# Kernel tuning notes

Measured on AMD Instinct MI355X. Metric: run time of the kernel, lower is better.

The kernel has to match this reference:

```python
import jax, jax.numpy as jnp
import numpy as np

B, S, HID = 1, 2048, 4096
NH, KVH, D = 32, 8, 128
MAXP = 2048
EPS = 1e-6


def _rope_tables(max_pos, dim, base=10000.0):
    inv_freq = 1.0 / (base ** (np.arange(0, dim, 2, dtype=np.float32) / dim))
    t = np.arange(max_pos, dtype=np.float32)
    freqs = np.outer(t, inv_freq)                      # [max_pos, dim/2]
    emb = np.concatenate([freqs, freqs], axis=-1)      # [max_pos, dim]
    return jnp.asarray(np.cos(emb)), jnp.asarray(np.sin(emb))


def setup_inputs() -> dict:
    key = jax.random.key(0)
    ks = jax.random.split(key, 6)
    x = jax.random.normal(ks[0], (B, S, HID), jnp.float32)
    scale = 0.02
    wq = jax.random.normal(ks[1], (NH * D, HID), jnp.float32) * scale
    wk = jax.random.normal(ks[2], (KVH * D, HID), jnp.float32) * scale
    wv = jax.random.normal(ks[3], (KVH * D, HID), jnp.float32) * scale
    wo = jax.random.normal(ks[4], (NH * D, HID), jnp.float32).T * scale  # stored as [HID, NH*D] -> transpose back
    wo = jnp.asarray(jax.random.normal(ks[4], (HID, NH * D), jnp.float32) * scale)
    cos_table, sin_table = _rope_tables(MAXP, D)
    return {
        "x": x, "wq": wq, "wk": wk, "wv": wv, "wo": wo,
        "q_norm_w": jnp.ones((D,), jnp.float32),
        "k_norm_w": jnp.ones((D,), jnp.float32),
        "cos_table": cos_table, "sin_table": sin_table,
        "k_cache": jnp.zeros((1, B, MAXP, KVH, D), jnp.float32),
        "v_cache": jnp.zeros((1, B, MAXP, KVH, D), jnp.float32),
        "positions": jnp.arange(S, dtype=jnp.int32),
        "layer_idx": 0,
    }


def _rmsnorm(x, w):
    return w * (x * jax.lax.rsqrt(jnp.mean(x * x, axis=-1, keepdims=True) + EPS))


def _rope(x, cos, sin):
    # x: [B, H, S, D]; cos/sin: [1, 1, S, D]
    half = x.shape[-1] // 2
    x1, x2 = x[..., :half], x[..., half:]
    rotated = jnp.concatenate([-x2, x1], axis=-1)
    return x * cos + rotated * sin


def reference(x, wq, wk, wv, wo, q_norm_w, k_norm_w, cos_table, sin_table,
              k_cache, v_cache, positions, layer_idx):
    bsz, seq_len, _ = x.shape
    d = q_norm_w.shape[0]
    nh = wq.shape[0] // d
    kvh = wk.shape[0] // d
    g = nh // kvh

    q = (x @ wq.T).reshape(bsz, seq_len, nh, d).transpose(0, 2, 1, 3)    # [B,NH,S,D]
    k = (x @ wk.T).reshape(bsz, seq_len, kvh, d).transpose(0, 2, 1, 3)   # [B,KVH,S,D]
    v = (x @ wv.T).reshape(bsz, seq_len, kvh, d).transpose(0, 2, 1, 3)

    q = _rmsnorm(q, q_norm_w)
    k = _rmsnorm(k, k_norm_w)

    cos = cos_table[positions][None, None]  # [1,1,S,D]
    sin = sin_table[positions][None, None]
    q = _rope(q, cos, sin)
    k = _rope(k, cos, sin)

    # KV-cache scatter at dynamic positions (prefill: positions = arange(S))
    kc = k_cache[layer_idx].at[:, positions].set(k.transpose(0, 2, 1, 3))
    vc = v_cache[layer_idx].at[:, positions].set(v.transpose(0, 2, 1, 3))
    # K = max(positions)+1 == seq_len in this (prefill) setup; static for jit
    K = seq_len
    k_all = kc[:, :K].transpose(0, 2, 1, 3)   # [B,KVH,K,D]
    v_all = vc[:, :K].transpose(0, 2, 1, 3)

    # GQA: group query heads instead of repeat_interleave on K/V (same math)
    qg = q.reshape(bsz, kvh, g, seq_len, d)
    scale = 1.0 / jnp.sqrt(jnp.asarray(d, q.dtype))
    scores = jnp.einsum('bkgqd,bkld->bkgql', qg, k_all) * scale
    causal = jnp.tril(jnp.ones((seq_len, K), dtype=bool))
    scores = jnp.where(causal, scores, jnp.finfo(scores.dtype).min)
    attn = jax.nn.softmax(scores, axis=-1)
    out = jnp.einsum('bkgql,bkld->bkgqd', attn, v_all)
    out = out.reshape(bsz, nh, seq_len, d).transpose(0, 2, 1, 3).reshape(bsz, seq_len, nh * d)
    return out @ wo.T
```

## Files before the change

kernel.cpp:

```cpp
#include <hip/hip_runtime.h>

typedef unsigned short u16;
typedef unsigned int u32;
typedef __attribute__((ext_vector_type(8))) short bf16x8;
typedef __attribute__((ext_vector_type(4))) float f32x4;
struct __align__(8) us4 { u16 x, y, z, w; };

#define S_LEN 2048
#define HID   4096
#define NH    32
#define KVH   8
#define HD    128
#define QP_ELEMS (S_LEN * HID)

__device__ inline u16 f2bf(float f) {
  u32 u = __float_as_uint(f);
  u32 r = (u + 0x7fffu + ((u >> 16) & 1u)) >> 16;
  return (u16)r;
}
__device__ inline float bf2f(u16 h) { return __uint_as_float(((u32)h) << 16); }

__device__ inline void gld_lds16(const void* g, void* l) {
  __builtin_amdgcn_global_load_lds(
      (const __attribute__((address_space(1))) u32*)g,
      (__attribute__((address_space(3))) u32*)l, 16, 0, 0);
}

__global__ __launch_bounds__(256)
void cvt_all(const float* __restrict__ x, const float* __restrict__ wq,
             const float* __restrict__ wk, const float* __restrict__ wv,
             const float* __restrict__ wo, u16* __restrict__ xb,
             u16* __restrict__ wqb, u16* __restrict__ wkb,
             u16* __restrict__ wvb, u16* __restrict__ wob) {
  int b = blockIdx.x;
  const float* in; u16* out; int base;
  if (b < 8192)       { in = x;  out = xb;  base = b; }
  else if (b < 24576) { in = wq; out = wqb; base = b - 8192; }
  else if (b < 28672) { in = wk; out = wkb; base = b - 24576; }
  else if (b < 32768) { in = wv; out = wvb; base = b - 28672; }
  else                { in = wo; out = wob; base = b - 32768; }
  size_t i = ((size_t)base * 256 + threadIdx.x) * 4;
  f32x4 v = *(const f32x4*)(in + i);
  us4 o;
  o.x = f2bf(v[0]); o.y = f2bf(v[1]); o.z = f2bf(v[2]); o.w = f2bf(v[3]);
  *(us4*)(out + i) = o;
}

__device__ inline void gemm_core_128(const u16* __restrict__ A,
                                     const u16* __restrict__ W,
                                     int m0, int n0, int K,
                                     int kStart, int kEnd,
                                     u16* lA, u16* lB, f32x4 (&acc)[4][4]) {
  const int t = threadIdx.x;
  const int l = t & 63, w = t >> 6;
  const int quad = l >> 4, l15 = l & 15;
  const int wr = w >> 1, wc = w & 1;
  const int srow = t >> 2;
  const int scol = (t & 3) * 8;
#pragma unroll
  for (int i = 0; i < 4; i++)
#pragma unroll
    for (int j = 0; j < 4; j++) acc[i][j] = (f32x4){0.f, 0.f, 0.f, 0.f};

  for (int k0 = kStart; k0 < kEnd; k0 += 32) {
    gld_lds16(A + (size_t)(m0 + srow) * K + k0 + scol, lA + srow * 32 + scol);
    gld_lds16(A + (size_t)(m0 + 64 + srow) * K + k0 + scol, lA + (64 + srow) * 32 + scol);
    gld_lds16(W + (size_t)(n0 + srow) * K + k0 + scol, lB + srow * 32 + scol);
    gld_lds16(W + (size_t)(n0 + 64 + srow) * K + k0 + scol, lB + (64 + srow) * 32 + scol);
    __syncthreads();
    bf16x8 af[4], bfr[4];
#pragma unroll
    for (int i = 0; i < 4; i++)
      af[i] = *(const bf16x8*)(lA + (wr * 64 + i * 16 + l15) * 32 + quad * 8);
#pragma unroll
    for (int j = 0; j < 4; j++)
      bfr[j] = *(const bf16x8*)(lB + (wc * 64 + j * 16 + l15) * 32 + quad * 8);
#pragma unroll
    for (int i = 0; i < 4; i++)
#pragma unroll
      for (int j = 0; j < 4; j++)
        acc[i][j] = __builtin_amdgcn_mfma_f32_16x16x32_bf16(af[i], bfr[j], acc[i][j], 0, 0, 0);
    __syncthreads();
  }
}

__global__ __launch_bounds__(256, 3)
void gemm_qkv(const u16* __restrict__ xb, const u16* __restrict__ wqb,
              const u16* __restrict__ wkb, const u16* __restrict__ wvb,
              u16* __restrict__ Qp, u16* __restrict__ Kp, u16* __restrict__ vt) {
  __shared__ __align__(16) u16 lA[128 * 32];
  __shared__ __align__(16) u16 lB[128 * 32];
  const int bx = blockIdx.x;
  const int m0 = blockIdx.y * 128;
  const u16* W; u16* C; int n0, ldc, epi;
  if (bx < 32)      { W = wqb; C = Qp; n0 = bx * 128;        ldc = HID;  epi = 0; }
  else if (bx < 40) { W = wkb; C = Kp; n0 = (bx - 32) * 128; ldc = 1024; epi = 0; }
  else              { W = wvb; C = vt; n0 = (bx - 40) * 128; ldc = 0;    epi = 1; }

  f32x4 acc[4][4];
  gemm_core_128(xb, W, m0, n0, HID, 0, HID, lA, lB, acc);

  const int t = threadIdx.x, l = t & 63, w = t >> 6;
  const int quad = l >> 4, l15 = l & 15;
  const int wr = w >> 1, wc = w & 1;
  if (epi == 0) {
#pragma unroll
    for (int i = 0; i < 4; i++) {
      int row0 = m0 + wr * 64 + i * 16 + quad * 4;
#pragma unroll
      for (int j = 0; j < 4; j++) {
        int col = n0 + wc * 64 + j * 16 + l15;
#pragma unroll
        for (int r = 0; r < 4; r++)
          C[(size_t)(row0 + r) * ldc + col] = f2bf(acc[i][j][r]);
      }
    }
  } else {
#pragma unroll
    for (int i = 0; i < 4; i++) {
      int row0 = m0 + wr * 64 + i * 16 + quad * 4;
#pragma unroll
      for (int j = 0; j < 4; j++) {
        int col = n0 + wc * 64 + j * 16 + l15;
        us4 v;
        v.x = f2bf(acc[i][j][0]); v.y = f2bf(acc[i][j][1]);
        v.z = f2bf(acc[i][j][2]); v.w = f2bf(acc[i][j][3]);
        *(us4*)(C + (size_t)col * S_LEN + row0) = v;
      }
    }
  }
}

__global__ __launch_bounds__(256, 3)
void gemm_out(const u16* __restrict__ ab, const u16* __restrict__ wob,
              u16* __restrict__ Po) {
  __shared__ __align__(16) u16 lA[128 * 32];
  __shared__ __align__(16) u16 lB[128 * 32];
  const int m0 = blockIdx.y * 128, n0 = blockIdx.x * 128;
  const int z = blockIdx.z;
  const int kStart = z * 1376;
  const int kEnd = (z == 2) ? HID : kStart + 1376;
  u16* C = Po + (size_t)z * QP_ELEMS;
  f32x4 acc[4][4];
  gemm_core_128(ab, wob, m0, n0, HID, kStart, kEnd, lA, lB, acc);
  const int t = threadIdx.x, l = t & 63, w = t >> 6;
  const int quad = l >> 4, l15 = l & 15;
  const int wr = w >> 1, wc = w & 1;
#pragma unroll
  for (int i = 0; i < 4; i++) {
    int row0 = m0 + wr * 64 + i * 16 + quad * 4;
#pragma unroll
    for (int j = 0; j < 4; j++) {
      int col = n0 + wc * 64 + j * 16 + l15;
#pragma unroll
      for (int r = 0; r < 4; r++)
        C[(size_t)(row0 + r) * HID + col] = f2bf(acc[i][j][r]);
    }
  }
}

__global__ __launch_bounds__(256)
void reduce_out(const u16* __restrict__ Po, float* __restrict__ outp) {
  size_t i = ((size_t)blockIdx.x * 256 + threadIdx.x) * 4;
  us4 a = *(const us4*)(Po + i);
  us4 b = *(const us4*)(Po + QP_ELEMS + i);
  us4 c = *(const us4*)(Po + 2 * QP_ELEMS + i);
  f32x4 o;
  o[0] = bf2f(a.x) + bf2f(b.x) + bf2f(c.x);
  o[1] = bf2f(a.y) + bf2f(b.y) + bf2f(c.y);
  o[2] = bf2f(a.z) + bf2f(b.z) + bf2f(c.z);
  o[3] = bf2f(a.w) + bf2f(b.w) + bf2f(c.w);
  *(f32x4*)(outp + i) = o;
}

__global__ __launch_bounds__(256)
void rope_all(const u16* __restrict__ Qp, const u16* __restrict__ Kp,
              const float* __restrict__ qnw, const float* __restrict__ knw,
              const float* __restrict__ cosT, const float* __restrict__ sinT,
              const int* __restrict__ pos, u16* __restrict__ qbh,
              u16* __restrict__ kbh) {
  const int b = blockIdx.x;
  const int t = threadIdx.x, w = t >> 6, l = t & 63;
  const u16* xr; const float* nw; u16* orow; int s;
  if (b < 16384) {
    int p = b * 4 + w;
    s = p >> 5; int h = p & 31;
    xr = Qp + (size_t)s * HID + h * HD;
    nw = qnw;
    orow = qbh + ((size_t)h * S_LEN + s) * HD;
  } else {
    int p = (b - 16384) * 4 + w;
    s = p >> 3; int h = p & 7;
    xr = Kp + (size_t)s * 1024 + h * HD;
    nw = knw;
    orow = kbh + ((size_t)h * S_LEN + s) * HD;
  }
  float x1 = bf2f(xr[l]);
  float x2 = bf2f(xr[l + 64]);
  float ss = x1 * x1 + x2 * x2;
#pragma unroll
  for (int m = 1; m < 64; m <<= 1) ss += __shfl_xor(ss, m);
  float rinv = rsqrtf(ss * (1.0f / 128.0f) + 1e-6f);
  float n1 = x1 * rinv * nw[l];
  float n2 = x2 * rinv * nw[l + 64];
  int ps = pos[s];
  float c1 = cosT[ps * HD + l], s1 = sinT[ps * HD + l];
  float c2 = cosT[ps * HD + l + 64], s2 = sinT[ps * HD + l + 64];
  float y1 = n1 * c1 - n2 * s1;
  float y2 = n2 * c2 + n1 * s2;
  orow[l] = f2bf(y1);
  orow[l + 64] = f2bf(y2);
}

__global__ __launch_bounds__(256)
void attn_fwd(const u16* __restrict__ qh, const u16* __restrict__ kbh,
              const u16* __restrict__ vth, u16* __restrict__ ab) {
  __shared__ __align__(16) u16 lK[64 * 128];
  __shared__ __align__(16) u16 lV[128 * 64];
  __shared__ __align__(16) u16 lP[4][16 * 72];
  const int t = threadIdx.x, w = t >> 6, l = t & 63;
  const int quad = l >> 4, l15 = l & 15;
  const int h = blockIdx.x;
  const int qt = 31 - blockIdx.y;
  const int kvh = h >> 2;
  const int q0 = qt * 64;
  const int qrow = q0 + w * 16 + l15;

  bf16x8 qf[4];
#pragma unroll
  for (int ks = 0; ks < 4; ks++)
    qf[ks] = *(const bf16x8*)(qh + ((size_t)h * S_LEN + qrow) * HD + ks * 32 + quad * 8);

  f32x4 accO[8];
#pragma unroll
  for (int j = 0; j < 8; j++) accO[j] = (f32x4){0.f, 0.f, 0.f, 0.f};
  float m_cur = -3.0e38f, l_sum = 0.f;
  const float scale2 = 0.12751743f;

  const int ntiles = qt + 1;
  for (int tt = 0; tt < ntiles; tt++) {
    const int c0 = tt * 64;
#pragma unroll
    for (int i = 0; i < 4; i++) {
      int Cc = i * 256 + t;
      int r = Cc >> 4, ch = Cc & 15;
      int gch = ch ^ (r & 15);
      gld_lds16(kbh + ((size_t)kvh * S_LEN + c0 + r) * HD + gch * 8, lK + Cc * 8);
    }
#pragma unroll
    for (int i = 0; i < 4; i++) {
      int Cc = i * 256 + t;
      int d = Cc >> 3, ch = Cc & 7;
      int gch = ch ^ (d & 7);
      gld_lds16(vth + ((size_t)kvh * HD + d) * S_LEN + c0 + gch * 8, lV + Cc * 8);
    }
    __syncthreads();

    f32x4 st[4];
#pragma unroll
    for (int i = 0; i < 4; i++) {
      f32x4 sa = (f32x4){0.f, 0.f, 0.f, 0.f};
      int r = i * 16 + l15;
#pragma unroll
      for (int ks = 0; ks < 4; ks++) {
        int lc = ks * 4 + quad;
        bf16x8 kf = *(const bf16x8*)(lK + r * 128 + ((lc ^ (r & 15)) * 8));
        sa = __builtin_amdgcn_mfma_f32_16x16x32_bf16(kf, qf[ks], sa, 0, 0, 0);
      }
      st[i] = sa;
    }

    const bool needMask = (c0 + 63) > (q0 + w * 16);
    float tmax = -3.0e38f;
    if (needMask) {
#pragma unroll
      for (int i = 0; i < 4; i++) {
#pragma unroll
        for (int r = 0; r < 4; r++) {
          int kcol = c0 + i * 16 + quad * 4 + r;
          float v = st[i][r] * scale2;
          v = (kcol <= qrow) ? v : -3.0e38f;
          st[i][r] = v;
          tmax = fmaxf(tmax, v);
        }
      }
    } else {
#pragma unroll
      for (int i = 0; i < 4; i++) {
#pragma unroll
        for (int r = 0; r < 4; r++) {
          float v = st[i][r] * scale2;
          st[i][r] = v;
          tmax = fmaxf(tmax, v);
        }
      }
    }
    tmax = fmaxf(tmax, __shfl_xor(tmax, 16));
    tmax = fmaxf(tmax, __shfl_xor(tmax, 32));
    float m_new = fmaxf(m_cur, tmax);
    float alpha = exp2f(m_cur - m_new);

    float psum = 0.f;
#pragma unroll
    for (int i = 0; i < 4; i++) {
      us4 pv;
      u16* pp = (u16*)&pv;
#pragma unroll
      for (int r = 0; r < 4; r++) {
        float pe = exp2f(st[i][r] - m_new);
        psum += pe;
        pp[r] = f2bf(pe);
      }
      *(us4*)(&lP[w][l15 * 72 + i * 16 + quad * 4]) = pv;
    }
    psum += __shfl_xor(psum, 16);
    psum += __shfl_xor(psum, 32);
    l_sum = l_sum * alpha + psum;
    m_cur = m_new;

#pragma unroll
    for (int r = 0; r < 4; r++) {
      float ar = __shfl(alpha, quad * 4 + r);
#pragma unroll
      for (int j = 0; j < 8; j++) accO[j][r] *= ar;
    }

    bf16x8 pf[2];
#pragma unroll
    for (int ks = 0; ks < 2; ks++)
      pf[ks] = *(const bf16x8*)(&lP[w][l15 * 72 + ks * 32 + quad * 8]);
#pragma unroll
    for (int j = 0; j < 8; j++) {
      int d = j * 16 + l15;
#pragma unroll
      for (int ks = 0; ks < 2; ks++) {
        int lc = ks * 4 + quad;
        bf16x8 vf = *(const bf16x8*)(lV + d * 64 + ((lc ^ (d & 7)) * 8));
        accO[j] = __builtin_amdgcn_mfma_f32_16x16x32_bf16(pf[ks], vf, accO[j], 0, 0, 0);
      }
    }
    __syncthreads();
  }

  float linv = 1.0f / l_sum;
#pragma unroll
  for (int r = 0; r < 4; r++) {
    float lr = __shfl(linv, quad * 4 + r);
    int row = q0 + w * 16 + quad * 4 + r;
#pragma unroll
    for (int j = 0; j < 8; j++) {
      int col = h * HD + j * 16 + l15;
      ab[(size_t)row * HID + col] = f2bf(accO[j][r] * lr);
    }
  }
}

extern "C" void kernel_launch(void* const* d_in, const int* in_sizes, int n_in,
                              void* d_out, int out_size, void* d_ws, size_t ws_size,
                              hipStream_t stream) {
  const float* x    = (const float*)d_in[0];
  const float* wq   = (const float*)d_in[1];
  const float* wk   = (const float*)d_in[2];
  const float* wv   = (const float*)d_in[3];
  const float* wo   = (const float*)d_in[4];
  const float* qnw  = (const float*)d_in[5];
  const float* knw  = (const float*)d_in[6];
  const float* cosT = (const float*)d_in[7];
  const float* sinT = (const float*)d_in[8];
  const int* positions = (const int*)d_in[11];

  char* ws = (char*)d_ws;
  const size_t MB = 1048576ULL;
  u16* xb  = (u16*)(ws + 0 * MB);
  u16* wqb = (u16*)(ws + 16 * MB);
  u16* wkb = (u16*)(ws + 48 * MB);
  u16* wvb = (u16*)(ws + 56 * MB);
  u16* wob = (u16*)(ws + 64 * MB);
  u16* Qp  = (u16*)(ws + 96 * MB);
  u16* Kp  = (u16*)(ws + 112 * MB);
  u16* vt  = (u16*)(ws + 116 * MB);
  u16* qbh = (u16*)(ws + 120 * MB);
  u16* kbh = (u16*)(ws + 136 * MB);
  u16* ab  = (u16*)(ws + 140 * MB);
  u16* Po  = (u16*)(ws + 0 * MB);

  cvt_all<<<49152, 256, 0, stream>>>(x, wq, wk, wv, wo, xb, wqb, wkb, wvb, wob);

  gemm_qkv<<<dim3(48, 16), 256, 0, stream>>>(xb, wqb, wkb, wvb, Qp, Kp, vt);

  rope_all<<<20480, 256, 0, stream>>>(Qp, Kp, qnw, knw, cosT, sinT, positions,
                                      qbh, kbh);

  attn_fwd<<<dim3(NH, S_LEN / 64), 256, 0, stream>>>(qbh, kbh, vt, ab);

  gemm_out<<<dim3(HID / 128, S_LEN / 128, 3), 256, 0, stream>>>(ab, wob, Po);
  reduce_out<<<8192, 256, 0, stream>>>(Po, (float*)d_out);
}
```

Before: 541.8 us.

## Double query rows per attention block to reuse K/V tiles across two MFMA sets

Each warp in the attention kernel now handles 32 query rows instead of 16, so a block covers a 128-row query tile and every K/V tile loaded into LDS feeds twice as many MFMAs. The grid shrinks to 512 one-dimensional blocks, and the query-tile order interleaves long and short causal rows so block lengths are spread out. The accumulator rescale is skipped when no lane's running max changed, and launch bounds ask for two blocks per CU. The cost is more accumulator registers per thread and fewer blocks to hide latency, and the diagonal tiles now do more masked wasted work.

Result: slower. 552.8 us (+2.0%).

```diff
diff --git a/kernel.cpp b/kernel.cpp
--- a/kernel.cpp
+++ b/kernel.cpp
@@ -212,145 +212,157 @@
   orow[l + 64] = f2bf(y2);
 }
 
-__global__ __launch_bounds__(256)
+__global__ __launch_bounds__(256, 2)
 void attn_fwd(const u16* __restrict__ qh, const u16* __restrict__ kbh,
               const u16* __restrict__ vth, u16* __restrict__ ab) {
   __shared__ __align__(16) u16 lK[64 * 128];
   __shared__ __align__(16) u16 lV[128 * 64];
-  __shared__ __align__(16) u16 lP[4][16 * 72];
+  __shared__ __align__(16) u16 lP[4][32 * 72];
   const int t = threadIdx.x, w = t >> 6, l = t & 63;
   const int quad = l >> 4, l15 = l & 15;
-  const int h = blockIdx.x;
-  const int qt = 31 - blockIdx.y;
+  const int h = blockIdx.x & 31;
+  const int iz = blockIdx.x >> 5;
+  const int qt = (iz < 8) ? (15 - iz) : (iz - 8);
   const int kvh = h >> 2;
-  const int q0 = qt * 64;
-  const int qrow = q0 + w * 16 + l15;
-
-  bf16x8 qf[4];
-#pragma unroll
-  for (int ks = 0; ks < 4; ks++)
-    qf[ks] = *(const bf16x8*)(qh + ((size_t)h * S_LEN + qrow) * HD + ks * 32 + quad * 8);
-
-  f32x4 accO[8];
-#pragma unroll
-  for (int j = 0; j < 8; j++) accO[j] = (f32x4){0.f, 0.f, 0.f, 0.f};
-  float m_cur = -3.0e38f, l_sum = 0.f;
+  const int q0 = qt * 128;
+  const int qb = q0 + w * 32;
+
+  bf16x8 qf[2][4];
+#pragma unroll
+  for (int nt = 0; nt < 2; nt++)
+#pragma unroll
+    for (int ks = 0; ks < 4; ks++)
+      qf[nt][ks] = *(const bf16x8*)(qh + ((size_t)h * S_LEN + qb + nt * 16 + l15) * HD +
+                                    ks * 32 + quad * 8);
+
+  f32x4 accO[2][8];
+#pragma unroll
+  for (int nt = 0; nt < 2; nt++)
+#pragma unroll
+    for (int j = 0; j < 8; j++) accO[nt][j] = (f32x4){0.f, 0.f, 0.f, 0.f};
+  float m_cur[2] = {-3.0e38f, -3.0e38f}, l_sum[2] = {0.f, 0.f};
   const float scale2 = 0.12751743f;
 
-  const int ntiles = qt + 1;
+  const int ntiles = 2 * qt + 2;
   for (int tt = 0; tt < ntiles; tt++) {
     const int c0 = tt * 64;
 #pragma unroll
     for (int i = 0; i < 4; i++) {
       int Cc = i * 256 + t;
       int r = Cc >> 4, ch = Cc & 15;
-      int gch = ch ^ (r & 15);
-      gld_lds16(kbh + ((size_t)kvh * S_LEN + c0 + r) * HD + gch * 8, lK + Cc * 8);
+      gld_lds16(kbh + ((size_t)kvh * S_LEN + c0 + r) * HD + (ch ^ (r & 15)) * 8, lK + Cc * 8);
     }
 #pragma unroll
     for (int i = 0; i < 4; i++) {
       int Cc = i * 256 + t;
       int d = Cc >> 3, ch = Cc & 7;
-      int gch = ch ^ (d & 7);
-      gld_lds16(vth + ((size_t)kvh * HD + d) * S_LEN + c0 + gch * 8, lV + Cc * 8);
+      gld_lds16(vth + ((size_t)kvh * HD + d) * S_LEN + c0 + (ch ^ (d & 7)) * 8, lV + Cc * 8);
     }
     __syncthreads();
 
-    f32x4 st[4];
+    f32x4 st[2][4];
 #pragma unroll
     for (int i = 0; i < 4; i++) {
-      f32x4 sa = (f32x4){0.f, 0.f, 0.f, 0.f};
+      f32x4 s0 = (f32x4){0.f, 0.f, 0.f, 0.f};
+      f32x4 s1 = (f32x4){0.f, 0.f, 0.f, 0.f};
       int r = i * 16 + l15;
 #pragma unroll
       for (int ks = 0; ks < 4; ks++) {
-        int lc = ks * 4 + quad;
-        bf16x8 kf = *(const bf16x8*)(lK + r * 128 + ((lc ^ (r & 15)) * 8));
-        sa = __builtin_amdgcn_mfma_f32_16x16x32_bf16(kf, qf[ks], sa, 0, 0, 0);
-      }
-      st[i] = sa;
-    }
-
-    const bool needMask = (c0 + 63) > (q0 + w * 16);
-    float tmax = -3.0e38f;
-    if (needMask) {
+        bf16x8 kf = *(const bf16x8*)(lK + r * 128 + (((ks * 4 + quad) ^ (r & 15)) * 8));
+        s0 = __builtin_amdgcn_mfma_f32_16x16x32_bf16(kf, qf[0][ks], s0, 0, 0, 0);
+        s1 = __builtin_amdgcn_mfma_f32_16x16x32_bf16(kf, qf[1][ks], s1, 0, 0, 0);
+      }
+      st[0][i] = s0; st[1][i] = s1;
+    }
+
+#pragma unroll
+    for (int nt = 0; nt < 2; nt++) {
+      const int qrow = qb + nt * 16 + l15;
+      const bool needMask = (c0 + 63) > (qb + nt * 16);
+      float tmax = -3.0e38f;
+      if (needMask) {
+#pragma unroll
+        for (int i = 0; i < 4; i++)
+#pragma unroll
+          for (int r = 0; r < 4; r++) {
+            int kcol = c0 + i * 16 + quad * 4 + r;
+            float v = st[nt][i][r] * scale2;
+            v = (kcol <= qrow) ? v : -3.0e38f;
+            st[nt][i][r] = v;
+            tmax = fmaxf(tmax, v);
+          }
+      } else {
+#pragma unroll
+        for (int i = 0; i < 4; i++)
+#pragma unroll
+          for (int r = 0; r < 4; r++) {
+            float v = st[nt][i][r] * scale2;
+            st[nt][i][r] = v;
+            tmax = fmaxf(tmax, v);
+          }
+      }
+      tmax = fmaxf(tmax, __shfl_xor(tmax, 16));
+      tmax = fmaxf(tmax, __shfl_xor(tmax, 32));
+      float m_new = fmaxf(m_cur[nt], tmax);
+      float alpha = exp2f(m_cur[nt] - m_new);
+
+      float psum = 0.f;
 #pragma unroll
       for (int i = 0; i < 4; i++) {
+        us4 pv;
+        u16* pp = (u16*)&pv;
 #pragma unroll
         for (int r = 0; r < 4; r++) {
-          int kcol = c0 + i * 16 + quad * 4 + r;
-          float v = st[i][r] * scale2;
-          v = (kcol <= qrow) ? v : -3.0e38f;
-          st[i][r] = v;
-          tmax = fmaxf(tmax, v);
+          float pe = exp2f(st[nt][i][r] - m_new);
+          psum += pe;
+          pp[r] = f2bf(pe);
         }
-      }
-    } else {
-#pragma unroll
-      for (int i = 0; i < 4; i++) {
+        *(us4*)(&lP[w][(nt * 16 + l15) * 72 + i * 16 + quad * 4]) = pv;
+      }
+      psum += __shfl_xor(psum, 16);
+      psum += __shfl_xor(psum, 32);
+      l_sum[nt] = l_sum[nt] * alpha + psum;
+      m_cur[nt] = m_new;
+
+      if (__ballot(alpha != 1.0f) != 0ULL) {
 #pragma unroll
         for (int r = 0; r < 4; r++) {
-          float v = st[i][r] * scale2;
-          st[i][r] = v;
-          tmax = fmaxf(tmax, v);
+          float ar = __shfl(alpha, quad * 4 + r);
+#pragma unroll
+          for (int j = 0; j < 8; j++) accO[nt][j][r] *= ar;
         }
       }
     }
-    tmax = fmaxf(tmax, __shfl_xor(tmax, 16));
-    tmax = fmaxf(tmax, __shfl_xor(tmax, 32));
-    float m_new = fmaxf(m_cur, tmax);
-    float alpha = exp2f(m_cur - m_new);
-
-    float psum = 0.f;
-#pragma unroll
-    for (int i = 0; i < 4; i++) {
-      us4 pv;
-      u16* pp = (u16*)&pv;
-#pragma unroll
-      for (int r = 0; r < 4; r++) {
-        float pe = exp2f(st[i][r] - m_new);
-        psum += pe;
-        pp[r] = f2bf(pe);
-      }
-      *(us4*)(&lP[w][l15 * 72 + i * 16 + quad * 4]) = pv;
-    }
-    psum += __shfl_xor(psum, 16);
-    psum += __shfl_xor(psum, 32);
-    l_sum = l_sum * alpha + psum;
-    m_cur = m_new;
-
-#pragma unroll
-    for (int r = 0; r < 4; r++) {
-      float ar = __shfl(alpha, quad * 4 + r);
-#pragma unroll
-      for (int j = 0; j < 8; j++) accO[j][r] *= ar;
-    }
-
-    bf16x8 pf[2];
-#pragma unroll
-    for (int ks = 0; ks < 2; ks++)
-      pf[ks] = *(const bf16x8*)(&lP[w][l15 * 72 + ks * 32 + quad * 8]);
+
+    bf16x8 pf[2][2];
+#pragma unroll
+    for (int nt = 0; nt < 2; nt++)
+#pragma unroll
+      for (int ks = 0; ks < 2; ks++)
+        pf[nt][ks] = *(const bf16x8*)(&lP[w][(nt * 16 + l15) * 72 + ks * 32 + quad * 8]);
 #pragma unroll
     for (int j = 0; j < 8; j++) {
       int d = j * 16 + l15;
 #pragma unroll
       for (int ks = 0; ks < 2; ks++) {
-        int lc = ks * 4 + quad;
-        bf16x8 vf = *(const bf16x8*)(lV + d * 64 + ((lc ^ (d & 7)) * 8));
-        accO[j] = __builtin_amdgcn_mfma_f32_16x16x32_bf16(pf[ks], vf, accO[j], 0, 0, 0);
+        bf16x8 vf = *(const bf16x8*)(lV + d * 64 + (((ks * 4 + quad) ^ (d & 7)) * 8));
+        accO[0][j] = __builtin_amdgcn_mfma_f32_16x16x32_bf16(pf[0][ks], vf, accO[0][j], 0, 0, 0);
+        accO[1][j] = __builtin_amdgcn_mfma_f32_16x16x32_bf16(pf[1][ks], vf, accO[1][j], 0, 0, 0);
       }
     }
     __syncthreads();
   }
 
-  float linv = 1.0f / l_sum;
-#pragma unroll
-  for (int r = 0; r < 4; r++) {
-    float lr = __shfl(linv, quad * 4 + r);
-    int row = q0 + w * 16 + quad * 4 + r;
-#pragma unroll
-    for (int j = 0; j < 8; j++) {
-      int col = h * HD + j * 16 + l15;
-      ab[(size_t)row * HID + col] = f2bf(accO[j][r] * lr);
+#pragma unroll
+  for (int nt = 0; nt < 2; nt++) {
+    float linv = 1.0f / l_sum[nt];
+#pragma unroll
+    for (int r = 0; r < 4; r++) {
+      float lr = __shfl(linv, quad * 4 + r);
+      int row = qb + nt * 16 + quad * 4 + r;
+#pragma unroll
+      for (int j = 0; j < 8; j++)
+        ab[(size_t)row * HID + h * HD + j * 16 + l15] = f2bf(accO[nt][j][r] * lr);
     }
   }
 }
@@ -391,7 +403,7 @@
   rope_all<<<20480, 256, 0, stream>>>(Qp, Kp, qnw, knw, cosT, sinT, positions,
                                       qbh, kbh);
 
-  attn_fwd<<<dim3(NH, S_LEN / 64), 256, 0, stream>>>(qbh, kbh, vt, ab);
+  attn_fwd<<<512, 256, 0, stream>>>(qbh, kbh, vt, ab);
 
   gemm_out<<<dim3(HID / 128, S_LEN / 128, 3), 256, 0, stream>>>(ab, wob, Po);
   reduce_out<<<8192, 256, 0, stream>>>(Po, (float*)d_out);
```
